# Kernel tuning notes

Hardware: AMD Instinct MI355X
Metric: run time of the kernel (lower is better)

Reference implementation:

```python
import jax, jax.numpy as jnp
import numpy as np

# ---- fixed kernels (match kornia.filters.canny defaults) ----
_POS = [(1, 2), (2, 2), (2, 1), (2, 0), (1, 0), (0, 0), (0, 1), (0, 2)]  # 8 directions, 45deg steps
_nms = np.zeros((8, 1, 3, 3), np.float32)
_hyst = np.zeros((8, 1, 3, 3), np.float32)
for _i, (_r, _c) in enumerate(_POS):
    _nms[_i, 0, 1, 1] = 1.0
    _nms[_i, 0, _r, _c] = -1.0
    _hyst[_i, 0, _r, _c] = 1.0
NMS_K = jnp.asarray(_nms)
HYST_K = jnp.asarray(_hyst)
SOBEL_X = jnp.asarray(np.array([[-1, 0, 1], [-2, 0, 2], [-1, 0, 1]], np.float32).reshape(1, 1, 3, 3))
SOBEL_Y = jnp.asarray(np.array([[-1, -2, -1], [0, 0, 0], [1, 2, 1]], np.float32).reshape(1, 1, 3, 3))


def _conv(x, w, pad):
    return jax.lax.conv_general_dilated(x, w, (1, 1), [(pad, pad), (pad, pad)],
                                        dimension_numbers=('NCHW', 'OIHW', 'NCHW'))


def _gauss_blur(x):
    # 5x5 gaussian, sigma=1, reflect padding (kornia gaussian_blur2d defaults)
    t = jnp.arange(5, dtype=x.dtype) - 2.0
    g = jnp.exp(-0.5 * t * t)
    g = g / g.sum()
    xp = jnp.pad(x, ((0, 0), (0, 0), (2, 2), (2, 2)), mode='reflect')
    x = _conv(xp, g.reshape(1, 1, 5, 1), 0)
    return _conv(x, g.reshape(1, 1, 1, 5), 0)


def canny_edges(img, low=0.1, high=0.2, eps=1e-6):
    # img: (N, 1, H, W) grayscale stack
    b = _gauss_blur(img)
    bp = jnp.pad(b, ((0, 0), (0, 0), (1, 1), (1, 1)), mode='edge')  # replicate pad for sobel
    gx = _conv(bp, SOBEL_X, 0)
    gy = _conv(bp, SOBEL_Y, 0)
    mag = jnp.sqrt(gx * gx + gy * gy + eps)                  # (N,1,H,W)
    ang = jnp.round(jnp.arctan2(gy, gx) * (180.0 / np.pi) / 45.0)  # in {-4..4}
    # angle-dependent non-max suppression via 8 directional difference kernels
    nmsv = _conv(mag, NMS_K, 1)                               # (N,8,H,W)
    pos = jnp.mod(ang, 8).astype(jnp.int32)
    neg = jnp.mod(ang + 4, 8).astype(jnp.int32)
    sp = jnp.take_along_axis(nmsv, pos, axis=1)
    sn = jnp.take_along_axis(nmsv, neg, axis=1)
    mag = mag * (jnp.minimum(sp, sn) > 0.0)
    # double threshold: weak=0.5, strong=1.0
    edges = (mag > low).astype(mag.dtype) * 0.5 + (mag > high) * 0.5

    # hysteresis: iterate until fixed point (weak pixels touching strong become strong)
    def cond(c):
        return ~jnp.all(c[0] == c[1])

    def body(c):
        e, _ = c
        weak = (e == 0.5).astype(e.dtype)
        strong = (e == 1.0).astype(e.dtype)
        hm = jnp.any(_conv(e, HYST_K, 1) == 1.0, axis=1, keepdims=True).astype(e.dtype)
        hm = hm * weak + strong
        return hm + (hm == 0) * weak * 0.5, e

    edges, _ = jax.lax.while_loop(cond, body, (edges, -jnp.ones_like(edges)))
    return edges


def setup_inputs() -> dict:
    key = jax.random.key(0)
    k1, k2 = jax.random.split(key)
    x = jax.random.normal(k1, (1, 64, 512, 512), dtype=jnp.float32)
    params = jnp.ones((1,), dtype=jnp.int64)
    indices = jax.random.randint(k2, (32,), 0, 64, dtype=jnp.int64)
    return {'x': x, 'params': params, 'indices': indices}


def reference(x, params, indices):
    if int(params[0]) == 0:
        return x
    sel = jnp.transpose(x, (1, 0, 2, 3))[indices]        # (K, 1, H, W)
    tf = canny_edges(sel)                                 # (K, 1, H, W) in {0, 0.5, 1}
    return x[:, indices] * jnp.transpose(tf, (1, 0, 2, 3))
```

## Files before the change

### kernel.cpp

```cpp
#include <hip/hip_runtime.h>
#include <cstdint>
#include <math.h>

#pragma clang fp contract(off)


constexpr int HH = 512;
constexpr int WW = 512;
constexpr int HW = HH * WW;
constexpr int KCH = 32;
constexpr int WORDS = HW / 32;

constexpr int TD = 32;
constexpr int NT = HH / TD;

constexpr int IN_D = TD + 8;
constexpr int VP_R = TD + 4;
constexpr int VP_C = TD + 8;
constexpr int BL_D = TD + 4;
constexpr int SQ_D = TD + 2;

constexpr double E2 = 0.13533528323661269189;
constexpr double E1 = 0.60653065971263342360;
constexpr double GS = ((((E2 + E1) + 1.0) + E1) + E2);
constexpr double GW0 = E2 / GS, GW1 = E1 / GS, GW2 = 1.0 / GS;

constexpr double T1 = 0.4142135623730950488;
constexpr double T2 = 2.4142135623730950488;

constexpr double SQ_HI = 0.2 * 0.2;
constexpr double SQ_LO = 0.1 * 0.1;

__device__ __forceinline__ int reflect_idx(int v) {
    return v < 0 ? -v : (v > 511 ? 1022 - v : v);
}
__device__ __forceinline__ int clampi(int v) {
    return v < 0 ? 0 : (v > 511 ? 511 : v);
}

__device__ const int AY1[4] = {0, 1, 1, 1};
__device__ const int AX1[4] = {1, 1, 0, -1};

__global__ __launch_bounds__(256) void canny_fused(const float* __restrict__ x,
                                                   const int* __restrict__ idx,
                                                   unsigned int* __restrict__ weakb,
                                                   unsigned int* __restrict__ strongb) {
    #pragma clang fp contract(off)
    __shared__ __align__(16) char lds[22912];
    double* vp_s = (double*)lds;
    double* sq_s = (double*)lds;
    double* bl_s = (double*)(lds + 11520);
    float*  in_s = (float*)(lds + 11520);
    unsigned char* ax_s = (unsigned char*)(lds + 21888);

    int tile = blockIdx.x;
    int k = tile >> 8;
    int t = tile & 255;
    int ty0 = (t >> 4) * TD;
    int tx0 = (t & 15) * TD;
    int tid = threadIdx.x;

    int ch = idx[k];
    const float* img = x + (size_t)ch * HW;

    for (int i = tid; i < IN_D * IN_D; i += 256) {
        int a = i / IN_D, b = i - a * IN_D;
        int gy = reflect_idx(ty0 - 4 + a);
        int gx = reflect_idx(tx0 - 4 + b);
        in_s[i] = img[gy * WW + gx];
    }
    __syncthreads();

    const double g[5] = {GW0, GW1, GW2, GW1, GW0};

    for (int c = tid; c < VP_R * VP_C; c += 256) {
        int a = c / VP_C, b = c - a * VP_C;
        double acc = 0.0;
        #pragma unroll
        for (int j = 0; j < 5; j++) {
            acc += g[j] * (double)in_s[(a + j) * IN_D + b];
        }
        vp_s[c] = acc;
    }
    __syncthreads();

    for (int c = tid; c < BL_D * BL_D; c += 256) {
        int a = c / BL_D, b = c - a * BL_D;
        double acc = 0.0;
        #pragma unroll
        for (int i = 0; i < 5; i++) {
            acc += g[i] * vp_s[a * VP_C + b + i];
        }
        bl_s[c] = acc;
    }
    __syncthreads();

    for (int c = tid; c < SQ_D * SQ_D; c += 256) {
        int am = c / SQ_D, bm = c - am * SQ_D;
        int u = ty0 - 1 + am, v = tx0 - 1 + bm;
        int ru = clampi(u - 1) - (ty0 - 2);
        int r0 = am + 1;
        int rd = clampi(u + 1) - (ty0 - 2);
        int cl = clampi(v - 1) - (tx0 - 2);
        int c0 = bm + 1;
        int cr = clampi(v + 1) - (tx0 - 2);
        double v00 = bl_s[ru * BL_D + cl], v01 = bl_s[ru * BL_D + c0], v02 = bl_s[ru * BL_D + cr];
        double v10 = bl_s[r0 * BL_D + cl],                              v12 = bl_s[r0 * BL_D + cr];
        double v20 = bl_s[rd * BL_D + cl], v21 = bl_s[rd * BL_D + c0], v22 = bl_s[rd * BL_D + cr];
        double gxv = ((((-v00 + v02) + (-2.0 * v10)) + (2.0 * v12)) + (-v20)) + v22;
        double gyv = ((((-v00 + (-2.0 * v01)) + (-v02)) + v20) + (2.0 * v21)) + v22;
        sq_s[c] = (gxv * gxv + gyv * gyv) + 1e-6;

        double axv = fabs(gxv), ayv = fabs(gyv);
        int axis;
        if (ayv < T1 * axv) axis = 0;
        else if (ayv > T2 * axv) axis = 2;
        else {
            double gxf = (gyv < 0.0) ? -gxv : gxv;
            axis = (gxf > 0.0) ? 1 : 3;
        }
        if (am >= 1 && am <= TD && bm >= 1 && bm <= TD)
            ax_s[(am - 1) * TD + (bm - 1)] = (unsigned char)axis;
    }
    __syncthreads();

    for (int q4 = 0; q4 < TD * TD / 256; q4++) {
        int l = q4 * 256 + tid;
        int oy = l >> 5, ox = l & 31;
        int gy = ty0 + oy, gx = tx0 + ox;

        int axis = ax_s[oy * TD + ox];
        int dy = AY1[axis], dx = AX1[axis];
        double s = sq_s[(oy + 1) * SQ_D + (ox + 1)];

        int y1 = gy + dy, x1 = gx + dx;
        int y2 = gy - dy, x2 = gx - dx;
        double s1 = (y1 >= 0 && y1 < HH && x1 >= 0 && x1 < WW)
                        ? sq_s[(oy + 1 + dy) * SQ_D + (ox + 1 + dx)] : 0.0;
        double s2 = (y2 >= 0 && y2 < HH && x2 >= 0 && x2 < WW)
                        ? sq_s[(oy + 1 - dy) * SQ_D + (ox + 1 - dx)] : 0.0;
        bool keep = (s > s1) && (s > s2);

        bool strong = keep && (s > SQ_HI);
        bool weak = keep && (s > SQ_LO) && !strong;

        unsigned long long wb = __ballot(weak);
        unsigned long long sb = __ballot(strong);
        if ((tid & 31) == 0) {
            unsigned int ww = (tid & 32) ? (unsigned int)(wb >> 32) : (unsigned int)wb;
            unsigned int sw = (tid & 32) ? (unsigned int)(sb >> 32) : (unsigned int)sb;
            size_t w32 = ((size_t)k * HW + (size_t)gy * WW + tx0) >> 5;
            weakb[w32] = ww;
            strongb[w32] = sw;
        }
    }
}

__global__ __launch_bounds__(1024) void hyst_iterate(const unsigned int* __restrict__ weakb,
                                                     unsigned int* __restrict__ strongb) {
    int k = blockIdx.x;
    __shared__ unsigned int Sm[WORDS];
    __shared__ int s_changed;
    int tid = threadIdx.x;

    const unsigned int* wsrc = weakb + (size_t)k * WORDS;
    unsigned int* ssrc = strongb + (size_t)k * WORDS;

    if (tid == 0) s_changed = 0;
    for (int i = tid; i < WORDS; i += 1024) Sm[i] = ssrc[i];
    unsigned int wreg[8];
    #pragma unroll
    for (int q = 0; q < 8; q++) wreg[q] = wsrc[tid * 8 + q];
    __syncthreads();

    for (;;) {
        int loc = 0;
        #pragma unroll
        for (int q = 0; q < 8; q++) {
            int w = tid * 8 + q;
            unsigned int s = Sm[w];
            unsigned int wk = wreg[q] & ~s;
            if (!wk) continue;
            int j = w & 15;
            unsigned int L = j ? Sm[w - 1] : 0u;
            unsigned int R = (j < 15) ? Sm[w + 1] : 0u;
            unsigned int D = (s << 1) | (L >> 31) | (s >> 1) | (R << 31);
            if (w >= 16) {
                unsigned int cu = Sm[w - 16];
                unsigned int Lu = j ? Sm[w - 17] : 0u;
                unsigned int Ru = (j < 15) ? Sm[w - 15] : 0u;
                D |= cu | (cu << 1) | (Lu >> 31) | (cu >> 1) | (Ru << 31);
            }
            if (w < WORDS - 16) {
                unsigned int cd = Sm[w + 16];
                unsigned int Ld = j ? Sm[w + 15] : 0u;
                unsigned int Rd = (j < 15) ? Sm[w + 17] : 0u;
                D |= cd | (cd << 1) | (Ld >> 31) | (cd >> 1) | (Rd << 31);
            }
            unsigned int promoted = wk & D;
            if (promoted) { Sm[w] = s | promoted; loc = 1; }
        }
        if (loc) s_changed = 1;
        __syncthreads();
        int chg = s_changed;
        __syncthreads();
        if (!chg) break;
        if (tid == 0) s_changed = 0;
        __syncthreads();
    }

    for (int i = tid; i < WORDS; i += 1024) ssrc[i] = Sm[i];
}

__global__ void mul_kernel(const float* __restrict__ x,
                           const int* __restrict__ idx,
                           const unsigned int* __restrict__ weakb,
                           const unsigned int* __restrict__ strongb,
                           float* __restrict__ out) {
    int gid = blockIdx.x * blockDim.x + threadIdx.x;
    int p = gid * 4;
    if (p >= KCH * HW) return;
    int k = p >> 18;
    int r = p & (HW - 1);
    int ch = idx[k];

    unsigned int sw = strongb[p >> 5];
    unsigned int ww = weakb[p >> 5];
    int b0 = p & 31;

    const float4 xv = *reinterpret_cast<const float4*>(x + (size_t)ch * HW + r);
    float t[4];
    #pragma unroll
    for (int i = 0; i < 4; i++) {
        int b = b0 + i;
        t[i] = ((sw >> b) & 1u) ? 1.0f : (((ww >> b) & 1u) ? 0.5f : 0.0f);
    }
    float4 o;
    o.x = xv.x * t[0];
    o.y = xv.y * t[1];
    o.z = xv.z * t[2];
    o.w = xv.w * t[3];
    *reinterpret_cast<float4*>(out + (size_t)p) = o;
}

extern "C" void kernel_launch(void* const* d_in, const int* in_sizes, int n_in,
                              void* d_out, int out_size, void* d_ws, size_t ws_size,
                              hipStream_t stream) {
    const float* x = (const float*)d_in[0];
    const int* idx = (const int*)d_in[2];
    float* out = (float*)d_out;

    char* ws = (char*)d_ws;
    unsigned int* weakb = (unsigned int*)ws;
    unsigned int* strongb = (unsigned int*)(ws + 1048576);

    int ntiles = KCH * NT * NT;
    canny_fused<<<ntiles, 256, 0, stream>>>(x, idx, weakb, strongb);
    hyst_iterate<<<KCH, 1024, 0, stream>>>(weakb, strongb);
    mul_kernel<<<(KCH * HW / 4) / 256, 256, 0, stream>>>(x, idx, weakb, strongb, out);
}
```

Before: 71.11 us.

## Register-block the Gaussian passes and precompute reflect/clamp index tables

Replaces the per-element 5-tap vertical and horizontal Gaussian loops with register-blocked versions, where each thread loads a 10-element window into registers and produces six outputs. This cuts redundant shared-memory loads. Reflect and clamp index computations move into small LDS lookup tables filled once per block. The strided loops also drop per-iteration integer division in favour of incremental index stepping. FP contraction is re-enabled, which allows FMA fusion but may change rounding of the double-precision arithmetic relative to the reference.

After: 69.28 us. 2.6% less time.

```diff
diff --git a/kernel.cpp b/kernel.cpp
--- a/kernel.cpp
+++ b/kernel.cpp
@@ -2,7 +2,6 @@
 #include <cstdint>
 #include <math.h>
 
-#pragma clang fp contract(off)
 
 
 constexpr int HH = 512;
@@ -14,11 +13,10 @@
 constexpr int TD = 32;
 constexpr int NT = HH / TD;
 
-constexpr int IN_D = TD + 8;
-constexpr int VP_R = TD + 4;
-constexpr int VP_C = TD + 8;
-constexpr int BL_D = TD + 4;
-constexpr int SQ_D = TD + 2;
+constexpr int IN_D = 40;
+constexpr int VP_R = 36, VP_C = 40;
+constexpr int BL_D = 36;
+constexpr int SQ_D = 34;
 
 constexpr double E2 = 0.13533528323661269189;
 constexpr double E1 = 0.60653065971263342360;
@@ -45,13 +43,18 @@
                                                    const int* __restrict__ idx,
                                                    unsigned int* __restrict__ weakb,
                                                    unsigned int* __restrict__ strongb) {
-    #pragma clang fp contract(off)
-    __shared__ __align__(16) char lds[22912];
+    __shared__ __align__(16) char lds[23296];
     double* vp_s = (double*)lds;
     double* sq_s = (double*)lds;
+    float*  in_s = (float*)(lds + 11520);
     double* bl_s = (double*)(lds + 11520);
-    float*  in_s = (float*)(lds + 11520);
     unsigned char* ax_s = (unsigned char*)(lds + 21888);
+    unsigned char* RUm = (unsigned char*)(lds + 22912);
+    unsigned char* RDm = RUm + 34;
+    unsigned char* CLm = RUm + 68;
+    unsigned char* CRm = RUm + 102;
+    unsigned short* rmap = (unsigned short*)(lds + 23048);
+    unsigned short* cmap = rmap + 40;
 
     int tile = blockIdx.x;
     int k = tile >> 8;
@@ -63,67 +66,102 @@
     int ch = idx[k];
     const float* img = x + (size_t)ch * HW;
 
-    for (int i = tid; i < IN_D * IN_D; i += 256) {
-        int a = i / IN_D, b = i - a * IN_D;
-        int gy = reflect_idx(ty0 - 4 + a);
-        int gx = reflect_idx(tx0 - 4 + b);
-        in_s[i] = img[gy * WW + gx];
+    if (tid < 40) {
+        rmap[tid] = (unsigned short)reflect_idx(ty0 - 4 + tid);
+        cmap[tid] = (unsigned short)reflect_idx(tx0 - 4 + tid);
+    } else if (tid >= 64 && tid < 98) {
+        int am = tid - 64;
+        int u = ty0 - 1 + am;
+        RUm[am] = (unsigned char)(clampi(u - 1) - (ty0 - 2));
+        RDm[am] = (unsigned char)(clampi(u + 1) - (ty0 - 2));
+    } else if (tid >= 128 && tid < 162) {
+        int bm = tid - 128;
+        int v = tx0 - 1 + bm;
+        CLm[bm] = (unsigned char)(clampi(v - 1) - (tx0 - 2));
+        CRm[bm] = (unsigned char)(clampi(v + 1) - (tx0 - 2));
+    }
+    __syncthreads();
+
+    {
+        int a = tid / 40, b = tid - a * 40;
+        while (a < 40) {
+            in_s[a * IN_D + b] = img[(int)rmap[a] * WW + (int)cmap[b]];
+            b += 16; a += 6;
+            if (b >= 40) { b -= 40; a += 1; }
+        }
     }
     __syncthreads();
 
     const double g[5] = {GW0, GW1, GW2, GW1, GW0};
 
-    for (int c = tid; c < VP_R * VP_C; c += 256) {
-        int a = c / VP_C, b = c - a * VP_C;
-        double acc = 0.0;
-        #pragma unroll
-        for (int j = 0; j < 5; j++) {
-            acc += g[j] * (double)in_s[(a + j) * IN_D + b];
-        }
-        vp_s[c] = acc;
-    }
-    __syncthreads();
-
-    for (int c = tid; c < BL_D * BL_D; c += 256) {
-        int a = c / BL_D, b = c - a * BL_D;
-        double acc = 0.0;
-        #pragma unroll
-        for (int i = 0; i < 5; i++) {
-            acc += g[i] * vp_s[a * VP_C + b + i];
-        }
-        bl_s[c] = acc;
-    }
-    __syncthreads();
-
-    for (int c = tid; c < SQ_D * SQ_D; c += 256) {
-        int am = c / SQ_D, bm = c - am * SQ_D;
-        int u = ty0 - 1 + am, v = tx0 - 1 + bm;
-        int ru = clampi(u - 1) - (ty0 - 2);
-        int r0 = am + 1;
-        int rd = clampi(u + 1) - (ty0 - 2);
-        int cl = clampi(v - 1) - (tx0 - 2);
-        int c0 = bm + 1;
-        int cr = clampi(v + 1) - (tx0 - 2);
-        double v00 = bl_s[ru * BL_D + cl], v01 = bl_s[ru * BL_D + c0], v02 = bl_s[ru * BL_D + cr];
-        double v10 = bl_s[r0 * BL_D + cl],                              v12 = bl_s[r0 * BL_D + cr];
-        double v20 = bl_s[rd * BL_D + cl], v21 = bl_s[rd * BL_D + c0], v22 = bl_s[rd * BL_D + cr];
-        double gxv = ((((-v00 + v02) + (-2.0 * v10)) + (2.0 * v12)) + (-v20)) + v22;
-        double gyv = ((((-v00 + (-2.0 * v01)) + (-v02)) + v20) + (2.0 * v21)) + v22;
-        sq_s[c] = (gxv * gxv + gyv * gyv) + 1e-6;
-
-        double axv = fabs(gxv), ayv = fabs(gyv);
-        int axis;
-        if (ayv < T1 * axv) axis = 0;
-        else if (ayv > T2 * axv) axis = 2;
-        else {
-            double gxf = (gyv < 0.0) ? -gxv : gxv;
-            axis = (gxf > 0.0) ? 1 : 3;
-        }
-        if (am >= 1 && am <= TD && bm >= 1 && bm <= TD)
-            ax_s[(am - 1) * TD + (bm - 1)] = (unsigned char)axis;
-    }
-    __syncthreads();
-
+    if (tid < 240) {
+        int b = tid / 6;
+        int r = tid - 6 * b;
+        int a0 = 6 * r;
+        double w[10];
+        #pragma unroll
+        for (int j = 0; j < 10; j++) w[j] = (double)in_s[(a0 + j) * IN_D + b];
+        #pragma unroll
+        for (int i = 0; i < 6; i++) {
+            double acc = g[0] * w[i];
+            acc += g[1] * w[i + 1];
+            acc += g[2] * w[i + 2];
+            acc += g[3] * w[i + 3];
+            acc += g[4] * w[i + 4];
+            vp_s[(a0 + i) * VP_C + b] = acc;
+        }
+    }
+    __syncthreads();
+
+    if (tid < 216) {
+        int a = tid / 6;
+        int q = tid - 6 * a;
+        int c0 = 6 * q;
+        double w[10];
+        #pragma unroll
+        for (int j = 0; j < 10; j++) w[j] = vp_s[a * VP_C + c0 + j];
+        #pragma unroll
+        for (int m = 0; m < 6; m++) {
+            double acc = g[0] * w[m];
+            acc += g[1] * w[m + 1];
+            acc += g[2] * w[m + 2];
+            acc += g[3] * w[m + 3];
+            acc += g[4] * w[m + 4];
+            bl_s[a * BL_D + c0 + m] = acc;
+        }
+    }
+    __syncthreads();
+
+    {
+        int am = tid / 34, bm = tid - 34 * am;
+        while (am < 34) {
+            int ru = RUm[am], r0 = am + 1, rd = RDm[am];
+            int cl = CLm[bm], c0 = bm + 1, cr = CRm[bm];
+            double v00 = bl_s[ru * BL_D + cl], v01 = bl_s[ru * BL_D + c0], v02 = bl_s[ru * BL_D + cr];
+            double v10 = bl_s[r0 * BL_D + cl],                              v12 = bl_s[r0 * BL_D + cr];
+            double v20 = bl_s[rd * BL_D + cl], v21 = bl_s[rd * BL_D + c0], v22 = bl_s[rd * BL_D + cr];
+            double gxv = ((((-v00 + v02) + (-2.0 * v10)) + (2.0 * v12)) + (-v20)) + v22;
+            double gyv = ((((-v00 + (-2.0 * v01)) + (-v02)) + v20) + (2.0 * v21)) + v22;
+            sq_s[am * SQ_D + bm] = (gxv * gxv + gyv * gyv) + 1e-6;
+
+            double axv = fabs(gxv), ayv = fabs(gyv);
+            int axis;
+            if (ayv < T1 * axv) axis = 0;
+            else if (ayv > T2 * axv) axis = 2;
+            else {
+                double gxf = (gyv < 0.0) ? -gxv : gxv;
+                axis = (gxf > 0.0) ? 1 : 3;
+            }
+            if (am >= 1 && am <= TD && bm >= 1 && bm <= TD)
+                ax_s[(am - 1) * TD + (bm - 1)] = (unsigned char)axis;
+
+            bm += 18; am += 7;
+            if (bm >= 34) { bm -= 34; am += 1; }
+        }
+    }
+    __syncthreads();
+
+    #pragma unroll
     for (int q4 = 0; q4 < TD * TD / 256; q4++) {
         int l = q4 * 256 + tid;
         int oy = l >> 5, ox = l & 31;
```
